# Performance work log

Measured on AMD Instinct MI355X. Metric: run time of the kernel, lower is better.

## Reference

```python
import jax, jax.numpy as jnp
import numpy as np

NEMB = 128
N_NODES = 8192
N_EDGES = 16384
N_STEMS = 4096
N_GRAPHS = 256
N_BLOCKS = 105       # BlockDictionary.n_unique_blocks
N_STEMTYPES = 32     # BlockDictionary.n_stem_types
OUT_PER_STEM = 105
OUT_PER_STOP = 1
NUM_CONV_STEPS = 12
SLOPE = 0.01         # nn.LeakyReLU default negative slope


def _act(v):
    return jax.nn.leaky_relu(v, SLOPE)


def setup_inputs() -> dict:
    key = jax.random.key(0)
    ks = jax.random.split(key, 32)
    def p(i, shape, fan_in):
        return jax.random.normal(ks[i], shape, jnp.float32) / np.sqrt(fan_in).astype(np.float32)
    D = NEMB
    inp = {
        "x": jax.random.randint(ks[0], (N_NODES,), 0, N_BLOCKS + 1),
        "stemtypes": jax.random.randint(ks[1], (N_STEMS,), 0, N_STEMTYPES + 1),
        "edge_attr": jax.random.randint(ks[2], (N_EDGES, 2), 0, N_STEMTYPES),
        "edge_index": jax.random.randint(ks[3], (2, N_EDGES), 0, N_NODES),
        "stem_node_idx": jax.random.randint(ks[4], (N_STEMS,), 0, N_NODES),
        "node_batch": jnp.sort(jax.random.randint(ks[5], (N_NODES,), 0, N_GRAPHS)),
        # embedding tables
        "emb_block": p(6, (N_BLOCKS + 1, D), D),
        "emb_stem": p(7, (N_STEMTYPES + 1, D), D),
        "emb_bond": p(8, (N_STEMTYPES, D), D),
        # block2emb MLP
        "b2e_w1": p(9, (D, D), D), "b2e_b1": p(10, (D,), D),
        "b2e_w2": p(11, (D, D), D), "b2e_b2": p(12, (D,), D),
        # NNConv root weight + bias (edge-nn is identity: nn.Sequential())
        "conv_root": p(13, (D, D), D), "conv_bias": p(14, (D,), D),
        # GRU (torch gate order r, z, n)
        "gru_w_ih": p(15, (3 * D, D), D), "gru_w_hh": p(16, (3 * D, D), D),
        "gru_b_ih": p(17, (3 * D,), D), "gru_b_hh": p(18, (3 * D,), D),
        # stem2pred MLP (in = 2*D)
        "s2p_w1": p(19, (D, 2 * D), 2 * D), "s2p_b1": p(20, (D,), 2 * D),
        "s2p_w2": p(21, (D, D), D), "s2p_b2": p(22, (D,), D),
        "s2p_w3": p(23, (OUT_PER_STEM, D), D), "s2p_b3": p(24, (OUT_PER_STEM,), D),
        # global2pred MLP
        "g2p_w1": p(25, (D, D), D), "g2p_b1": p(26, (D,), D),
        "g2p_w2": p(27, (OUT_PER_STOP, D), D), "g2p_b2": p(28, (OUT_PER_STOP,), D),
    }
    return inp


def reference(x, stemtypes, edge_attr, edge_index, stem_node_idx, node_batch,
              emb_block, emb_stem, emb_bond,
              b2e_w1, b2e_b1, b2e_w2, b2e_b2,
              conv_root, conv_bias,
              gru_w_ih, gru_w_hh, gru_b_ih, gru_b_hh,
              s2p_w1, s2p_b1, s2p_w2, s2p_b2, s2p_w3, s2p_b3,
              g2p_w1, g2p_b1, g2p_w2, g2p_b2):
    block_emb = emb_block[x]                          # [N, D]
    stem_emb = emb_stem[stemtypes]                    # [S, D]
    be = emb_bond[edge_attr]                          # [E, 2, D]
    # outer product -> per-edge [D_in, D_out] weight (matches view(-1, in, out))
    W_e = be[:, 0, :, None] * be[:, 1, None, :]       # [E, D, D]

    out = _act(block_emb @ b2e_w1.T + b2e_b1) @ b2e_w2.T + b2e_b2  # [N, D]
    h = out                                           # GRU hidden state

    src, dst = edge_index[0], edge_index[1]
    ones_e = jnp.ones((N_EDGES,), out.dtype)
    deg = jax.ops.segment_sum(ones_e, dst, num_segments=N_NODES)
    inv_deg = jnp.where(deg > 0, 1.0 / jnp.maximum(deg, 1.0), 0.0)[:, None]

    for _ in range(NUM_CONV_STEPS):
        # NNConv: mean_j (x_j @ W_e) + x @ root + bias, then LeakyReLU
        msg = jnp.einsum('ei,eij->ej', out[src], W_e)                  # [E, D]
        agg = jax.ops.segment_sum(msg, dst, num_segments=N_NODES) * inv_deg
        m = _act(agg + out @ conv_root + conv_bias)
        # single-layer GRU, seq_len = 1
        gi = m @ gru_w_ih.T + gru_b_ih
        gh = h @ gru_w_hh.T + gru_b_hh
        ir, iz, inn = jnp.split(gi, 3, axis=-1)
        hr, hz, hn = jnp.split(gh, 3, axis=-1)
        r = jax.nn.sigmoid(ir + hr)
        z = jax.nn.sigmoid(iz + hz)
        n = jnp.tanh(inn + r * hn)
        h = (1.0 - z) * n + z * h
        out = h

    stem_cat = jnp.concatenate([out[stem_node_idx], stem_emb], axis=1)  # [S, 2D]
    s = _act(stem_cat @ s2p_w1.T + s2p_b1)
    s = _act(s @ s2p_w2.T + s2p_b2)
    stem_pred = s @ s2p_w3.T + s2p_b3                                   # [S, out_per_stem]

    # global_mean_pool
    gsum = jax.ops.segment_sum(out, node_batch, num_segments=N_GRAPHS)
    gcnt = jax.ops.segment_sum(jnp.ones((N_NODES,), out.dtype), node_batch, num_segments=N_GRAPHS)
    gmean = gsum / jnp.maximum(gcnt, 1.0)[:, None]
    g = _act(gmean @ g2p_w1.T + g2p_b1)
    stop_pred = g @ g2p_w2.T + g2p_b2                                   # [G, out_per_stop]
    return stem_pred, stop_pred
```

## Files before the change

kernel.cpp:

```cpp
#include <hip/hip_runtime.h>
#include <math.h>

#define D 128
#define NNODES 8192
#define NEDGES 16384
#define NSTEMS 4096
#define NGRAPHS 256
#define NSTEPS 12
#define OPS 105
#define SLOPE 0.01f
#define MT 32
#define NB (NNODES / MT)
#define ECAP 512
#define LDA 136
#define LDA2 264
#define LDQ2 34
#define LDH 132

typedef _Float16 half_t;
typedef __attribute__((ext_vector_type(8))) _Float16 f16x8;
typedef __attribute__((ext_vector_type(4))) float f32x4;

__device__ __forceinline__ float leaky(float x) { return x > 0.f ? x : SLOPE * x; }
__device__ __forceinline__ float fast_sigmoid(float x) {
    return __builtin_amdgcn_rcpf(1.f + __expf(-x));
}
__device__ __forceinline__ float fast_tanh(float x) {
    float e = __expf(2.f * x);
    return 1.f - 2.f * __builtin_amdgcn_rcpf(e + 1.f);
}

__device__ __forceinline__ void gbar_arrive(int* bar, int sync_no) {
    __syncthreads();
    if (threadIdx.x == 0) {
        int grp = blockIdx.x >> 4;
        int old = __hip_atomic_fetch_add(&bar[grp * 32], 1,
                                         __ATOMIC_RELEASE, __HIP_MEMORY_SCOPE_AGENT);
        if (old == sync_no * 16 - 1) {
            int r = __hip_atomic_fetch_add(&bar[512], 1,
                                           __ATOMIC_RELEASE, __HIP_MEMORY_SCOPE_AGENT);
            if (r == sync_no * 16 - 1)
                __hip_atomic_store(&bar[544], sync_no,
                                   __ATOMIC_RELEASE, __HIP_MEMORY_SCOPE_AGENT);
        }
    }
}
__device__ __forceinline__ void gbar_wait(int* bar, int sync_no) {
    if (threadIdx.x == 0) {
        while (__hip_atomic_load(&bar[544], __ATOMIC_RELAXED,
                                 __HIP_MEMORY_SCOPE_AGENT) < sync_no)
            __builtin_amdgcn_s_sleep(1);
    }
    __syncthreads();
}

__global__ void k_setup(
    const float* __restrict__ root, const float* __restrict__ wih,
    const float* __restrict__ whh, const float* __restrict__ bond,
    const float* __restrict__ sw1, const float* __restrict__ sw2,
    const float* __restrict__ sw3, const float* __restrict__ bw1,
    const float* __restrict__ bw2, const float* __restrict__ gw1,
    half_t* __restrict__ rootP, half_t* __restrict__ WihP,
    half_t* __restrict__ WhhP, half_t* __restrict__ bondTP,
    half_t* __restrict__ s1P, half_t* __restrict__ s2P, half_t* __restrict__ s3P,
    half_t* __restrict__ w1P, half_t* __restrict__ w2P, half_t* __restrict__ bondQP,
    float* __restrict__ g1T, int* __restrict__ zeroi) {
    int idx = blockIdx.x * 256 + threadIdx.x;
    int which = blockIdx.y;
    if (which == 10) {
        if (idx < 128 * 128) {
            int r = idx >> 7, c = idx & 127;
            g1T[c * 128 + r] = gw1[idx];
        }
        return;
    }
    if (which == 11) {
        if (idx < 1024) zeroi[idx] = 0;
        return;
    }
    int KT = (which == 4) ? 8 : (which == 9) ? 1 : 4;
    int NT = (which == 1 || which == 2) ? 24 : (which == 3) ? 2 : (which == 6) ? 7 : 8;
    if (idx >= NT * KT * 512) return;
    int j = idx & 7;
    int L = (idx >> 3) & 63;
    int t = idx >> 9;
    int kt = t % KT, nt = t / KT;
    int k = kt * 32 + (L >> 4) * 8 + j;
    int n = nt * 16 + (L & 15);
    switch (which) {
        case 0: rootP[idx] = (half_t)root[k * D + n]; break;
        case 1: WihP[idx] = (half_t)wih[n * D + k]; break;
        case 2: WhhP[idx] = (half_t)whh[n * D + k]; break;
        case 3: bondTP[idx] = (half_t)bond[n * D + k]; break;
        case 4: s1P[idx] = (half_t)sw1[n * 256 + k]; break;
        case 5: s2P[idx] = (half_t)sw2[n * 128 + k]; break;
        case 6: s3P[idx] = (n < OPS) ? (half_t)sw3[n * 128 + k] : (half_t)0.f; break;
        case 7: w1P[idx] = (half_t)bw1[n * D + k]; break;
        case 8: w2P[idx] = (half_t)bw2[n * D + k]; break;
        case 9: bondQP[idx] = (half_t)bond[k * D + n]; break;
    }
}

__device__ __forceinline__ int lower_bound_dev(const int* a, int n, int v) {
    int lo = 0, hi = n;
    while (lo < hi) {
        int m = (lo + hi) >> 1;
        if (a[m] < v) lo = m + 1;
        else hi = m;
    }
    return lo;
}

__global__ __launch_bounds__(512, 2) void k_fused(
    const int* __restrict__ x, const float* __restrict__ embBlock,
    const half_t* __restrict__ w1P, const float* __restrict__ b1i,
    const half_t* __restrict__ w2P, const float* __restrict__ b2i,
    const half_t* __restrict__ rootP, const half_t* __restrict__ WihP,
    const half_t* __restrict__ WhhP, const half_t* __restrict__ bondTP,
    const half_t* __restrict__ bondQP,
    const float* __restrict__ cbias, const float* __restrict__ bih,
    const float* __restrict__ bhh,
    const int* __restrict__ eidx, const int* __restrict__ eattr,
    float* __restrict__ Pbuf0, float* __restrict__ Pbuf1,
    float* __restrict__ hF,
    const int* __restrict__ sni, const int* __restrict__ stypes,
    const float* __restrict__ embStem,
    const half_t* __restrict__ s1P, const float* __restrict__ sb1,
    const half_t* __restrict__ s2P, const float* __restrict__ sb2,
    const half_t* __restrict__ s3P, const float* __restrict__ sb3,
    const int* __restrict__ batch, const float* __restrict__ g1T,
    const float* __restrict__ gb1, const float* __restrict__ gw2,
    const float* __restrict__ gb2, float* __restrict__ dout,
    int* __restrict__ bar) {
    __shared__ __align__(16) half_t As[MT * LDA];
    __shared__ __align__(16) half_t Am[MT * LDA];
    __shared__ __align__(16) float Hs[MT * LDH];
    __shared__ __align__(16) float Q[MT * LDQ2];
    __shared__ __align__(16) int4 elist[ECAP];
    __shared__ int degs_s[MT];
    __shared__ int ecnt;

    const int tid = threadIdx.x;
    const int w = tid >> 6;
    const int lane = tid & 63;
    const int quad = lane >> 4;
    const int l16 = lane & 15;
    const int n0 = blockIdx.x * MT;
    const int c = w * 16 + l16;

    if (tid < MT) degs_s[tid] = 0;
    if (tid == 0) ecnt = 0;
    for (int i = tid; i < MT * LDQ2; i += 512) Q[i] = 0.f;
    __syncthreads();

    {
        int row = tid >> 4;
        int col = (tid & 15) * 8;
        const float* src = embBlock + (size_t)x[n0 + row] * D + col;
        float4 v0 = ((const float4*)src)[0];
        float4 v1 = ((const float4*)src)[1];
        f16x8 hv;
        hv[0] = (half_t)v0.x; hv[1] = (half_t)v0.y; hv[2] = (half_t)v0.z; hv[3] = (half_t)v0.w;
        hv[4] = (half_t)v1.x; hv[5] = (half_t)v1.y; hv[6] = (half_t)v1.z; hv[7] = (half_t)v1.w;
        *(f16x8*)&As[row * LDA + col] = hv;
    }
    {
        const int4* dst4 = (const int4*)(eidx + NEDGES);
        for (int e4 = tid; e4 < NEDGES / 4; e4 += 512) {
            int4 dd = dst4[e4];
            int eb = e4 * 4;
            int dv[4] = {dd.x, dd.y, dd.z, dd.w};
#pragma unroll
            for (int q2 = 0; q2 < 4; ++q2) {
                unsigned r = (unsigned)(dv[q2] - n0);
                if (r < MT) {
                    int slot = atomicAdd(&ecnt, 1);
                    atomicAdd(&degs_s[r], 1);
                    if (slot < ECAP) {
                        int e = eb + q2;
                        int2 aa = *(const int2*)(eattr + 2 * e);
                        elist[slot] = make_int4(eidx[e], aa.x, aa.y, (int)r);
                    }
                }
            }
        }
    }
    f16x8 rootB[4], ghB[12], giB[12], aggB, bondTB[4];
#pragma unroll
    for (int kt = 0; kt < 4; ++kt)
        rootB[kt] = *(const f16x8*)(rootP + (size_t)((w * 4 + kt) * 64 + lane) * 8);
#pragma unroll
    for (int kt = 0; kt < 4; ++kt)
#pragma unroll
        for (int g = 0; g < 3; ++g)
            ghB[g * 4 + kt] = *(const f16x8*)(WhhP + (size_t)(((g * 8 + w) * 4 + kt) * 64 + lane) * 8);
#pragma unroll
    for (int kt = 0; kt < 4; ++kt)
#pragma unroll
        for (int g = 0; g < 3; ++g)
            giB[g * 4 + kt] = *(const f16x8*)(WihP + (size_t)(((g * 8 + w) * 4 + kt) * 64 + lane) * 8);
    aggB = *(const f16x8*)(bondQP + (size_t)(w * 64 + lane) * 8);
    {
        const int ntb = w & 1;
#pragma unroll
        for (int kt = 0; kt < 4; ++kt)
            bondTB[kt] = *(const f16x8*)(bondTP + (size_t)((ntb * 4 + kt) * 64 + lane) * 8);
    }
    const float cb = cbias[c];
    const float bi0 = bih[c], bi1 = bih[D + c], bi2 = bih[2 * D + c];
    const float bh0 = bhh[c], bh1 = bhh[D + c], bh2 = bhh[2 * D + c];
    __syncthreads();

    int4 ep = make_int4(0, 0, 0, 0);
    float idg = 0.f;
    const int m = min(ecnt, ECAP);
    const bool have = (tid < m);
    if (have) {
        ep = elist[tid];
        idg = 1.0f / (float)degs_s[ep.w];
    }

    {
        f32x4 acc[2] = {{0.f, 0.f, 0.f, 0.f}, {0.f, 0.f, 0.f, 0.f}};
#pragma unroll
        for (int kt = 0; kt < 4; ++kt) {
            f16x8 b = *(const f16x8*)(w1P + (size_t)((w * 4 + kt) * 64 + lane) * 8);
            f16x8 a0 = *(const f16x8*)&As[(0 + l16) * LDA + kt * 32 + quad * 8];
            f16x8 a1 = *(const f16x8*)&As[(16 + l16) * LDA + kt * 32 + quad * 8];
            acc[0] = __builtin_amdgcn_mfma_f32_16x16x32_f16(a0, b, acc[0], 0, 0, 0);
            acc[1] = __builtin_amdgcn_mfma_f32_16x16x32_f16(a1, b, acc[1], 0, 0, 0);
        }
        float bb = b1i[c];
#pragma unroll
        for (int mt = 0; mt < 2; ++mt)
#pragma unroll
            for (int r = 0; r < 4; ++r)
                Am[(mt * 16 + quad * 4 + r) * LDA + c] = (half_t)leaky(acc[mt][r] + bb);
    }
    __syncthreads();
    {
        f32x4 acc[2] = {{0.f, 0.f, 0.f, 0.f}, {0.f, 0.f, 0.f, 0.f}};
#pragma unroll
        for (int kt = 0; kt < 4; ++kt) {
            f16x8 b = *(const f16x8*)(w2P + (size_t)((w * 4 + kt) * 64 + lane) * 8);
            f16x8 a0 = *(const f16x8*)&Am[(0 + l16) * LDA + kt * 32 + quad * 8];
            f16x8 a1 = *(const f16x8*)&Am[(16 + l16) * LDA + kt * 32 + quad * 8];
            acc[0] = __builtin_amdgcn_mfma_f32_16x16x32_f16(a0, b, acc[0], 0, 0, 0);
            acc[1] = __builtin_amdgcn_mfma_f32_16x16x32_f16(a1, b, acc[1], 0, 0, 0);
        }
        float bb = b2i[c];
#pragma unroll
        for (int mt = 0; mt < 2; ++mt)
#pragma unroll
            for (int r = 0; r < 4; ++r) {
                int row = mt * 16 + quad * 4 + r;
                float h = acc[mt][r] + bb;
                Hs[row * LDH + c] = h;
                As[row * LDA + c] = (half_t)h;
            }
    }
    __syncthreads();
    if (w < 4) {
        int mt = w >> 1;
        f32x4 acc = {0.f, 0.f, 0.f, 0.f};
#pragma unroll
        for (int kt = 0; kt < 4; ++kt) {
            f16x8 a = *(const f16x8*)&As[(mt * 16 + l16) * LDA + kt * 32 + quad * 8];
            acc = __builtin_amdgcn_mfma_f32_16x16x32_f16(a, bondTB[kt], acc, 0, 0, 0);
        }
#pragma unroll
        for (int r = 0; r < 4; ++r)
            __hip_atomic_store(
                &Pbuf0[(size_t)(n0 + mt * 16 + quad * 4 + r) * 32 + (w & 1) * 16 + l16],
                acc[r], __ATOMIC_RELAXED, __HIP_MEMORY_SCOPE_AGENT);
    }
    gbar_arrive(bar, 1);

    float* Pp = Pbuf0;
    float* Pn = Pbuf1;
    for (int step = 0; step < NSTEPS; ++step) {
        f32x4 ghA[2][3];
#pragma unroll
        for (int mt = 0; mt < 2; ++mt)
#pragma unroll
            for (int g = 0; g < 3; ++g) ghA[mt][g] = f32x4{0.f, 0.f, 0.f, 0.f};
#pragma unroll
        for (int kt = 0; kt < 4; ++kt) {
            f16x8 a0 = *(const f16x8*)&As[(0 + l16) * LDA + kt * 32 + quad * 8];
            f16x8 a1 = *(const f16x8*)&As[(16 + l16) * LDA + kt * 32 + quad * 8];
#pragma unroll
            for (int g = 0; g < 3; ++g) {
                ghA[0][g] = __builtin_amdgcn_mfma_f32_16x16x32_f16(a0, ghB[g * 4 + kt], ghA[0][g], 0, 0, 0);
                ghA[1][g] = __builtin_amdgcn_mfma_f32_16x16x32_f16(a1, ghB[g * 4 + kt], ghA[1][g], 0, 0, 0);
            }
        }
        gbar_wait(bar, step + 1);
        float wv = 0.f;
        if (have)
            wv = __hip_atomic_load(&Pp[(size_t)ep.x * 32 + ep.y],
                                   __ATOMIC_RELAXED, __HIP_MEMORY_SCOPE_AGENT) * idg;
        f32x4 convAcc[2] = {{0.f, 0.f, 0.f, 0.f}, {0.f, 0.f, 0.f, 0.f}};
#pragma unroll
        for (int kt = 0; kt < 4; ++kt) {
            f16x8 a0 = *(const f16x8*)&As[(0 + l16) * LDA + kt * 32 + quad * 8];
            f16x8 a1 = *(const f16x8*)&As[(16 + l16) * LDA + kt * 32 + quad * 8];
            convAcc[0] = __builtin_amdgcn_mfma_f32_16x16x32_f16(a0, rootB[kt], convAcc[0], 0, 0, 0);
            convAcc[1] = __builtin_amdgcn_mfma_f32_16x16x32_f16(a1, rootB[kt], convAcc[1], 0, 0, 0);
        }
        if (have) atomicAdd(&Q[ep.w * LDQ2 + ep.z], wv);
        __syncthreads();

#pragma unroll
        for (int mt = 0; mt < 2; ++mt) {
            const float* qrow = &Q[(mt * 16 + l16) * LDQ2 + quad * 8];
            f16x8 a;
#pragma unroll
            for (int jj = 0; jj < 8; ++jj) a[jj] = (half_t)qrow[jj];
            f32x4 acc = {0.f, 0.f, 0.f, 0.f};
            acc = __builtin_amdgcn_mfma_f32_16x16x32_f16(a, aggB, acc, 0, 0, 0);
#pragma unroll
            for (int r = 0; r < 4; ++r) {
                float mm = convAcc[mt][r] + cb + acc[r];
                Am[(mt * 16 + quad * 4 + r) * LDA + c] = (half_t)leaky(mm);
            }
        }
        __syncthreads();

        if (step < NSTEPS - 1)
            for (int i = tid; i < MT * LDQ2; i += 512) Q[i] = 0.f;
        f32x4 giA[2][3];
#pragma unroll
        for (int mt = 0; mt < 2; ++mt)
#pragma unroll
            for (int g = 0; g < 3; ++g) giA[mt][g] = f32x4{0.f, 0.f, 0.f, 0.f};
#pragma unroll
        for (int kt = 0; kt < 4; ++kt) {
            f16x8 a0 = *(const f16x8*)&Am[(0 + l16) * LDA + kt * 32 + quad * 8];
            f16x8 a1 = *(const f16x8*)&Am[(16 + l16) * LDA + kt * 32 + quad * 8];
#pragma unroll
            for (int g = 0; g < 3; ++g) {
                giA[0][g] = __builtin_amdgcn_mfma_f32_16x16x32_f16(a0, giB[g * 4 + kt], giA[0][g], 0, 0, 0);
                giA[1][g] = __builtin_amdgcn_mfma_f32_16x16x32_f16(a1, giB[g * 4 + kt], giA[1][g], 0, 0, 0);
            }
        }
#pragma unroll
        for (int mt = 0; mt < 2; ++mt) {
#pragma unroll
            for (int r = 0; r < 4; ++r) {
                int row = mt * 16 + quad * 4 + r;
                float rg = fast_sigmoid(giA[mt][0][r] + bi0 + ghA[mt][0][r] + bh0);
                float z = fast_sigmoid(giA[mt][1][r] + bi1 + ghA[mt][1][r] + bh1);
                float nn = fast_tanh(giA[mt][2][r] + bi2 + rg * (ghA[mt][2][r] + bh2));
                float hnew = (1.f - z) * nn + z * Hs[row * LDH + c];
                Hs[row * LDH + c] = hnew;
                As[row * LDA + c] = (half_t)hnew;
            }
        }
        __syncthreads();

        if (step < NSTEPS - 1) {
            if (w < 4) {
                int mt = w >> 1;
                f32x4 acc = {0.f, 0.f, 0.f, 0.f};
#pragma unroll
                for (int kt = 0; kt < 4; ++kt) {
                    f16x8 a = *(const f16x8*)&As[(mt * 16 + l16) * LDA + kt * 32 + quad * 8];
                    acc = __builtin_amdgcn_mfma_f32_16x16x32_f16(a, bondTB[kt], acc, 0, 0, 0);
                }
#pragma unroll
                for (int r = 0; r < 4; ++r)
                    __hip_atomic_store(
                        &Pn[(size_t)(n0 + mt * 16 + quad * 4 + r) * 32 + (w & 1) * 16 + l16],
                        acc[r], __ATOMIC_RELAXED, __HIP_MEMORY_SCOPE_AGENT);
            }
            gbar_arrive(bar, step + 2);
            float* tsw = Pp; Pp = Pn; Pn = tsw;
        }
    }

    half_t* cat = As;
    half_t* t1 = Am;
    half_t* t2 = Am + 16 * LDA;
    const int s0 = blockIdx.x * 16;
    {
        int row = tid >> 4;
        int col = (tid & 15) * 8;
        const unsigned long long* s8 = (const unsigned long long*)&Hs[row * LDH + col];
        unsigned long long* d8 = (unsigned long long*)(hF + (size_t)(n0 + row) * D + col);
#pragma unroll
        for (int q2 = 0; q2 < 4; ++q2)
            __hip_atomic_store(d8 + q2, s8[q2], __ATOMIC_RELAXED, __HIP_MEMORY_SCOPE_AGENT);
    }
    if (tid < 256) {
        int row = tid >> 4;
        int col = (tid & 15) * 8;
        const float* src = embStem + (size_t)stypes[s0 + row] * D + col;
        float4 v0 = ((const float4*)src)[0];
        float4 v1 = ((const float4*)src)[1];
        f16x8 hv;
        hv[0] = (half_t)v0.x; hv[1] = (half_t)v0.y; hv[2] = (half_t)v0.z; hv[3] = (half_t)v0.w;
        hv[4] = (half_t)v1.x; hv[5] = (half_t)v1.y; hv[6] = (half_t)v1.z; hv[7] = (half_t)v1.w;
        *(f16x8*)&cat[row * LDA2 + 128 + col] = hv;
    }
    gbar_arrive(bar, NSTEPS + 1);

    f32x4 accS = {0.f, 0.f, 0.f, 0.f};
#pragma unroll
    for (int kt = 4; kt < 8; ++kt) {
        f16x8 b = *(const f16x8*)(s1P + (size_t)((w * 8 + kt) * 64 + lane) * 8);
        f16x8 a = *(const f16x8*)&cat[l16 * LDA2 + kt * 32 + quad * 8];
        accS = __builtin_amdgcn_mfma_f32_16x16x32_f16(a, b, accS, 0, 0, 0);
    }
    gbar_wait(bar, NSTEPS + 1);

    if (tid < 256) {
        int row = tid >> 4;
        int col = (tid & 15) * 8;
        const float* src = hF + (size_t)sni[s0 + row] * D + col;
        float4 v0 = ((const float4*)src)[0];
        float4 v1 = ((const float4*)src)[1];
        f16x8 hv;
        hv[0] = (half_t)v0.x; hv[1] = (half_t)v0.y; hv[2] = (half_t)v0.z; hv[3] = (half_t)v0.w;
        hv[4] = (half_t)v1.x; hv[5] = (half_t)v1.y; hv[6] = (half_t)v1.z; hv[7] = (half_t)v1.w;
        *(f16x8*)&cat[row * LDA2 + col] = hv;
    }
    __syncthreads();
    {
#pragma unroll
        for (int kt = 0; kt < 4; ++kt) {
            f16x8 b = *(const f16x8*)(s1P + (size_t)((w * 8 + kt) * 64 + lane) * 8);
            f16x8 a = *(const f16x8*)&cat[l16 * LDA2 + kt * 32 + quad * 8];
            accS = __builtin_amdgcn_mfma_f32_16x16x32_f16(a, b, accS, 0, 0, 0);
        }
        float bb = sb1[c];
#pragma unroll
        for (int r = 0; r < 4; ++r)
            t1[(quad * 4 + r) * LDA + c] = (half_t)leaky(accS[r] + bb);
    }
    __syncthreads();
    {
        f32x4 acc = {0.f, 0.f, 0.f, 0.f};
#pragma unroll
        for (int kt = 0; kt < 4; ++kt) {
            f16x8 b = *(const f16x8*)(s2P + (size_t)((w * 4 + kt) * 64 + lane) * 8);
            f16x8 a = *(const f16x8*)&t1[l16 * LDA + kt * 32 + quad * 8];
            acc = __builtin_amdgcn_mfma_f32_16x16x32_f16(a, b, acc, 0, 0, 0);
        }
        float bb = sb2[c];
#pragma unroll
        for (int r = 0; r < 4; ++r)
            t2[(quad * 4 + r) * LDA + c] = (half_t)leaky(acc[r] + bb);
    }
    __syncthreads();
    if (w < 7) {
        f32x4 acc = {0.f, 0.f, 0.f, 0.f};
#pragma unroll
        for (int kt = 0; kt < 4; ++kt) {
            f16x8 b = *(const f16x8*)(s3P + (size_t)((w * 4 + kt) * 64 + lane) * 8);
            f16x8 a = *(const f16x8*)&t2[l16 * LDA + kt * 32 + quad * 8];
            acc = __builtin_amdgcn_mfma_f32_16x16x32_f16(a, b, acc, 0, 0, 0);
        }
        int j = w * 16 + l16;
        if (j < OPS) {
            float bb = sb3[j];
#pragma unroll
            for (int r = 0; r < 4; ++r)
                dout[(size_t)(s0 + quad * 4 + r) * OPS + j] = acc[r] + bb;
        }
    }

    {
        const int g = blockIdx.x;
        const int j = tid & 127;
        const int grp = tid >> 7;
        float* part = Q;
        float* mean_s = Q + 512;
        float* red = Q + 640;
        int lo = lower_bound_dev(batch, NNODES, g);
        int hi = lower_bound_dev(batch, NNODES, g + 1);
        float sum = 0.f;
        for (int n = lo + grp; n < hi; n += 4) sum += hF[(size_t)n * D + j];
        part[grp * 128 + j] = sum;
        __syncthreads();
        if (grp == 0) {
            float denom = (hi > lo) ? (float)(hi - lo) : 1.0f;
            mean_s[j] = (part[j] + part[128 + j] + part[256 + j] + part[384 + j]) / denom;
        }
        __syncthreads();
        float a = 0.f;
        for (int i = grp * 32; i < grp * 32 + 32; ++i) a += mean_s[i] * g1T[i * D + j];
        part[grp * 128 + j] = a;
        __syncthreads();
        if (grp == 0) {
            float aa = part[j] + part[128 + j] + part[256 + j] + part[384 + j] + gb1[j];
            red[j] = leaky(aa) * gw2[j];
        }
        __syncthreads();
        for (int off = 64; off > 0; off >>= 1) {
            if (tid < off) red[tid] += red[tid + off];
            __syncthreads();
        }
        if (tid == 0) dout[NSTEMS * OPS + g] = red[0] + gb2[0];
    }
}

extern "C" void kernel_launch(void* const* d_in, const int* in_sizes, int n_in,
                              void* d_out, int out_size, void* d_ws, size_t ws_size,
                              hipStream_t stream) {
    const int* x = (const int*)d_in[0];
    const int* stypes = (const int*)d_in[1];
    const int* eattr = (const int*)d_in[2];
    const int* eidx = (const int*)d_in[3];
    const int* sni = (const int*)d_in[4];
    const int* batch = (const int*)d_in[5];
    const float* embBlock = (const float*)d_in[6];
    const float* embStem = (const float*)d_in[7];
    const float* embBond = (const float*)d_in[8];
    const float* b2e_w1 = (const float*)d_in[9];
    const float* b2e_b1 = (const float*)d_in[10];
    const float* b2e_w2 = (const float*)d_in[11];
    const float* b2e_b2 = (const float*)d_in[12];
    const float* conv_root = (const float*)d_in[13];
    const float* conv_bias = (const float*)d_in[14];
    const float* gru_w_ih = (const float*)d_in[15];
    const float* gru_w_hh = (const float*)d_in[16];
    const float* gru_b_ih = (const float*)d_in[17];
    const float* gru_b_hh = (const float*)d_in[18];
    const float* s2p_w1 = (const float*)d_in[19];
    const float* s2p_b1 = (const float*)d_in[20];
    const float* s2p_w2 = (const float*)d_in[21];
    const float* s2p_b2 = (const float*)d_in[22];
    const float* s2p_w3 = (const float*)d_in[23];
    const float* s2p_b3 = (const float*)d_in[24];
    const float* g2p_w1 = (const float*)d_in[25];
    const float* g2p_b1 = (const float*)d_in[26];
    const float* g2p_w2 = (const float*)d_in[27];
    const float* g2p_b2 = (const float*)d_in[28];
    float* out_f = (float*)d_out;

    float* W = (float*)d_ws;
    size_t off = 0;
    auto alloc = [&](size_t words) {
        size_t o = off;
        off += (words + 3) & ~(size_t)3;
        return o;
    };
    float* hF = W + alloc(NNODES * D);
    float* P0 = W + alloc(NNODES * 32);
    float* P1 = W + alloc(NNODES * 32);
    half_t* rootP = (half_t*)(W + alloc(16384 / 2));
    half_t* WihP = (half_t*)(W + alloc(49152 / 2));
    half_t* WhhP = (half_t*)(W + alloc(49152 / 2));
    half_t* bondTP = (half_t*)(W + alloc(4096 / 2));
    half_t* s1P = (half_t*)(W + alloc(32768 / 2));
    half_t* s2P = (half_t*)(W + alloc(16384 / 2));
    half_t* s3P = (half_t*)(W + alloc(14336 / 2));
    half_t* w1P = (half_t*)(W + alloc(16384 / 2));
    half_t* w2P = (half_t*)(W + alloc(16384 / 2));
    half_t* bondQP = (half_t*)(W + alloc(4096 / 2));
    float* g1T = W + alloc(128 * 128);
    int* bar = (int*)(W + alloc(1024));

    k_setup<<<dim3(192, 12), 256, 0, stream>>>(
        conv_root, gru_w_ih, gru_w_hh, embBond, s2p_w1, s2p_w2, s2p_w3,
        b2e_w1, b2e_w2, g2p_w1,
        rootP, WihP, WhhP, bondTP, s1P, s2P, s3P, w1P, w2P, bondQP,
        g1T, bar);

    k_fused<<<NB, 512, 0, stream>>>(
        x, embBlock,
        w1P, b2e_b1, w2P, b2e_b2,
        rootP, WihP, WhhP, bondTP, bondQP,
        conv_bias, gru_b_ih, gru_b_hh,
        eidx, eattr,
        P0, P1, hF,
        sni, stypes, embStem,
        s1P, s2p_b1, s2P, s2p_b2, s3P, s2p_b3,
        batch, g1T, g2p_b1, g2p_w2, g2p_b2,
        out_f, bar);
}
```

Measured before the change: 219.8 us.

## Switch message passing from pull-gather to push-scatter with global atomics

Edges are now grouped by source node. Each block computes its nodes' projected messages in shared memory and atomically adds them, already scaled by inverse degree, into a double-buffered global aggregation array owned by the destination node. Each block then reads its own 32x32 aggregate slice contiguously and zeroes it for reuse. This replaces scattered per-edge remote loads after the barrier with atomics issued before the barrier, so the post-barrier critical path becomes one coalesced load. In exchange it adds an extra grid barrier to publish inverse degrees, more global atomic traffic, and a zeroing pass in setup.

```diff
diff --git a/kernel.cpp b/kernel.cpp
--- a/kernel.cpp
+++ b/kernel.cpp
@@ -64,7 +64,7 @@
     half_t* __restrict__ WhhP, half_t* __restrict__ bondTP,
     half_t* __restrict__ s1P, half_t* __restrict__ s2P, half_t* __restrict__ s3P,
     half_t* __restrict__ w1P, half_t* __restrict__ w2P, half_t* __restrict__ bondQP,
-    float* __restrict__ g1T, int* __restrict__ zeroi) {
+    float* __restrict__ g1T, int* __restrict__ zeroi, float* __restrict__ Qg) {
     int idx = blockIdx.x * 256 + threadIdx.x;
     int which = blockIdx.y;
     if (which == 10) {
@@ -76,6 +76,10 @@
     }
     if (which == 11) {
         if (idx < 1024) zeroi[idx] = 0;
+        return;
+    }
+    if (which == 12) {
+        for (int i = idx; i < 2 * NNODES * 32; i += 192 * 256) Qg[i] = 0.f;
         return;
     }
     int KT = (which == 4) ? 8 : (which == 9) ? 1 : 4;
@@ -121,7 +125,7 @@
     const float* __restrict__ cbias, const float* __restrict__ bih,
     const float* __restrict__ bhh,
     const int* __restrict__ eidx, const int* __restrict__ eattr,
-    float* __restrict__ Pbuf0, float* __restrict__ Pbuf1,
+    float* __restrict__ Qg, float* __restrict__ invDegG,
     float* __restrict__ hF,
     const int* __restrict__ sni, const int* __restrict__ stypes,
     const float* __restrict__ embStem,
@@ -135,7 +139,7 @@
     __shared__ __align__(16) half_t As[MT * LDA];
     __shared__ __align__(16) half_t Am[MT * LDA];
     __shared__ __align__(16) float Hs[MT * LDH];
-    __shared__ __align__(16) float Q[MT * LDQ2];
+    __shared__ __align__(16) float QPs[MT * LDQ2];
     __shared__ __align__(16) int4 elist[ECAP];
     __shared__ int degs_s[MT];
     __shared__ int ecnt;
@@ -150,7 +154,6 @@
 
     if (tid < MT) degs_s[tid] = 0;
     if (tid == 0) ecnt = 0;
-    for (int i = tid; i < MT * LDQ2; i += 512) Q[i] = 0.f;
     __syncthreads();
 
     {
@@ -165,21 +168,25 @@
         *(f16x8*)&As[row * LDA + col] = hv;
     }
     {
-        const int4* dst4 = (const int4*)(eidx + NEDGES);
+        const int4* src4p = (const int4*)eidx;
+        const int4* dst4p = (const int4*)(eidx + NEDGES);
         for (int e4 = tid; e4 < NEDGES / 4; e4 += 512) {
-            int4 dd = dst4[e4];
+            int4 ss = src4p[e4];
+            int4 dd = dst4p[e4];
             int eb = e4 * 4;
+            int sv[4] = {ss.x, ss.y, ss.z, ss.w};
             int dv[4] = {dd.x, dd.y, dd.z, dd.w};
 #pragma unroll
             for (int q2 = 0; q2 < 4; ++q2) {
-                unsigned r = (unsigned)(dv[q2] - n0);
-                if (r < MT) {
+                unsigned rd = (unsigned)(dv[q2] - n0);
+                if (rd < MT) atomicAdd(&degs_s[rd], 1);
+                unsigned rs = (unsigned)(sv[q2] - n0);
+                if (rs < MT) {
                     int slot = atomicAdd(&ecnt, 1);
-                    atomicAdd(&degs_s[r], 1);
                     if (slot < ECAP) {
                         int e = eb + q2;
                         int2 aa = *(const int2*)(eattr + 2 * e);
-                        elist[slot] = make_int4(eidx[e], aa.x, aa.y, (int)r);
+                        elist[slot] = make_int4((int)rs, aa.x, aa.y, dv[q2]);
                     }
                 }
             }
@@ -211,14 +218,16 @@
     const float bh0 = bhh[c], bh1 = bhh[D + c], bh2 = bhh[2 * D + c];
     __syncthreads();
 
+    if (tid < MT) {
+        int dg = degs_s[tid];
+        __hip_atomic_store(&invDegG[n0 + tid], dg > 0 ? 1.0f / (float)dg : 0.0f,
+                           __ATOMIC_RELAXED, __HIP_MEMORY_SCOPE_AGENT);
+    }
     int4 ep = make_int4(0, 0, 0, 0);
-    float idg = 0.f;
     const int m = min(ecnt, ECAP);
     const bool have = (tid < m);
-    if (have) {
-        ep = elist[tid];
-        idg = 1.0f / (float)degs_s[ep.w];
-    }
+    if (have) ep = elist[tid];
+    gbar_arrive(bar, 1);
 
     {
         f32x4 acc[2] = {{0.f, 0.f, 0.f, 0.f}, {0.f, 0.f, 0.f, 0.f}};
@@ -260,6 +269,10 @@
             }
     }
     __syncthreads();
+    gbar_wait(bar, 1);
+    float idg = 0.f;
+    if (have)
+        idg = __hip_atomic_load(&invDegG[ep.w], __ATOMIC_RELAXED, __HIP_MEMORY_SCOPE_AGENT);
     if (w < 4) {
         int mt = w >> 1;
         f32x4 acc = {0.f, 0.f, 0.f, 0.f};
@@ -270,14 +283,13 @@
         }
 #pragma unroll
         for (int r = 0; r < 4; ++r)
-            __hip_atomic_store(
-                &Pbuf0[(size_t)(n0 + mt * 16 + quad * 4 + r) * 32 + (w & 1) * 16 + l16],
-                acc[r], __ATOMIC_RELAXED, __HIP_MEMORY_SCOPE_AGENT);
-    }
-    gbar_arrive(bar, 1);
-
-    float* Pp = Pbuf0;
-    float* Pn = Pbuf1;
+            QPs[(mt * 16 + quad * 4 + r) * LDQ2 + (w & 1) * 16 + l16] = acc[r];
+    }
+    __syncthreads();
+    if (have)
+        atomicAdd(&Qg[(size_t)ep.w * 32 + ep.z], QPs[ep.x * LDQ2 + ep.y] * idg);
+    gbar_arrive(bar, 2);
+
     for (int step = 0; step < NSTEPS; ++step) {
         f32x4 ghA[2][3];
 #pragma unroll
@@ -294,11 +306,11 @@
                 ghA[1][g] = __builtin_amdgcn_mfma_f32_16x16x32_f16(a1, ghB[g * 4 + kt], ghA[1][g], 0, 0, 0);
             }
         }
-        gbar_wait(bar, step + 1);
-        float wv = 0.f;
-        if (have)
-            wv = __hip_atomic_load(&Pp[(size_t)ep.x * 32 + ep.y],
-                                   __ATOMIC_RELAXED, __HIP_MEMORY_SCOPE_AGENT) * idg;
+        gbar_wait(bar, step + 2);
+        float* Qc = Qg + (size_t)(step & 1) * (NNODES * 32) + (size_t)n0 * 32;
+        unsigned long long qv =
+            __hip_atomic_load((unsigned long long*)(Qc + tid * 2),
+                              __ATOMIC_RELAXED, __HIP_MEMORY_SCOPE_AGENT);
         f32x4 convAcc[2] = {{0.f, 0.f, 0.f, 0.f}, {0.f, 0.f, 0.f, 0.f}};
 #pragma unroll
         for (int kt = 0; kt < 4; ++kt) {
@@ -307,12 +319,20 @@
             convAcc[0] = __builtin_amdgcn_mfma_f32_16x16x32_f16(a0, rootB[kt], convAcc[0], 0, 0, 0);
             convAcc[1] = __builtin_amdgcn_mfma_f32_16x16x32_f16(a1, rootB[kt], convAcc[1], 0, 0, 0);
         }
-        if (have) atomicAdd(&Q[ep.w * LDQ2 + ep.z], wv);
+        {
+            union { unsigned long long u; float f[2]; } qu;
+            qu.u = qv;
+            int row = tid >> 4, col = (tid & 15) * 2;
+            QPs[row * LDQ2 + col] = qu.f[0];
+            QPs[row * LDQ2 + col + 1] = qu.f[1];
+            __hip_atomic_store((unsigned long long*)(Qc + tid * 2), 0ULL,
+                               __ATOMIC_RELAXED, __HIP_MEMORY_SCOPE_AGENT);
+        }
         __syncthreads();
 
 #pragma unroll
         for (int mt = 0; mt < 2; ++mt) {
-            const float* qrow = &Q[(mt * 16 + l16) * LDQ2 + quad * 8];
+            const float* qrow = &QPs[(mt * 16 + l16) * LDQ2 + quad * 8];
             f16x8 a;
 #pragma unroll
             for (int jj = 0; jj < 8; ++jj) a[jj] = (half_t)qrow[jj];
@@ -326,8 +346,6 @@
         }
         __syncthreads();
 
-        if (step < NSTEPS - 1)
-            for (int i = tid; i < MT * LDQ2; i += 512) Q[i] = 0.f;
         f32x4 giA[2][3];
 #pragma unroll
         for (int mt = 0; mt < 2; ++mt)
@@ -369,12 +387,14 @@
                 }
 #pragma unroll
                 for (int r = 0; r < 4; ++r)
-                    __hip_atomic_store(
-                        &Pn[(size_t)(n0 + mt * 16 + quad * 4 + r) * 32 + (w & 1) * 16 + l16],
-                        acc[r], __ATOMIC_RELAXED, __HIP_MEMORY_SCOPE_AGENT);
+                    QPs[(mt * 16 + quad * 4 + r) * LDQ2 + (w & 1) * 16 + l16] = acc[r];
             }
-            gbar_arrive(bar, step + 2);
-            float* tsw = Pp; Pp = Pn; Pn = tsw;
+            __syncthreads();
+            if (have)
+                atomicAdd(&Qg[(size_t)((step + 1) & 1) * (NNODES * 32) +
+                              (size_t)ep.w * 32 + ep.z],
+                          QPs[ep.x * LDQ2 + ep.y] * idg);
+            gbar_arrive(bar, step + 3);
         }
     }
 
@@ -402,7 +422,7 @@
         hv[4] = (half_t)v1.x; hv[5] = (half_t)v1.y; hv[6] = (half_t)v1.z; hv[7] = (half_t)v1.w;
         *(f16x8*)&cat[row * LDA2 + 128 + col] = hv;
     }
-    gbar_arrive(bar, NSTEPS + 1);
+    gbar_arrive(bar, NSTEPS + 2);
 
     f32x4 accS = {0.f, 0.f, 0.f, 0.f};
 #pragma unroll
@@ -411,7 +431,7 @@
         f16x8 a = *(const f16x8*)&cat[l16 * LDA2 + kt * 32 + quad * 8];
         accS = __builtin_amdgcn_mfma_f32_16x16x32_f16(a, b, accS, 0, 0, 0);
     }
-    gbar_wait(bar, NSTEPS + 1);
+    gbar_wait(bar, NSTEPS + 2);
 
     if (tid < 256) {
         int row = tid >> 4;
@@ -473,9 +493,9 @@
         const int g = blockIdx.x;
         const int j = tid & 127;
         const int grp = tid >> 7;
-        float* part = Q;
-        float* mean_s = Q + 512;
-        float* red = Q + 640;
+        float* part = QPs;
+        float* mean_s = QPs + 512;
+        float* red = QPs + 640;
         int lo = lower_bound_dev(batch, NNODES, g);
         int hi = lower_bound_dev(batch, NNODES, g + 1);
         float sum = 0.f;
@@ -546,8 +566,8 @@
         return o;
     };
     float* hF = W + alloc(NNODES * D);
-    float* P0 = W + alloc(NNODES * 32);
-    float* P1 = W + alloc(NNODES * 32);
+    float* Qg = W + alloc(2 * NNODES * 32);
+    float* invDegG = W + alloc(NNODES);
     half_t* rootP = (half_t*)(W + alloc(16384 / 2));
     half_t* WihP = (half_t*)(W + alloc(49152 / 2));
     half_t* WhhP = (half_t*)(W + alloc(49152 / 2));
@@ -561,11 +581,11 @@
     float* g1T = W + alloc(128 * 128);
     int* bar = (int*)(W + alloc(1024));
 
-    k_setup<<<dim3(192, 12), 256, 0, stream>>>(
+    k_setup<<<dim3(192, 13), 256, 0, stream>>>(
         conv_root, gru_w_ih, gru_w_hh, embBond, s2p_w1, s2p_w2, s2p_w3,
         b2e_w1, b2e_w2, g2p_w1,
         rootP, WihP, WhhP, bondTP, s1P, s2P, s3P, w1P, w2P, bondQP,
-        g1T, bar);
+        g1T, bar, Qg);
 
     k_fused<<<NB, 512, 0, stream>>>(
         x, embBlock,
@@ -573,7 +593,7 @@
         rootP, WihP, WhhP, bondTP, bondQP,
         conv_bias, gru_b_ih, gru_b_hh,
         eidx, eattr,
-        P0, P1, hF,
+        Qg, invDegG, hF,
         sni, stypes, embStem,
         s1P, s2p_b1, s2P, s2p_b2, s3P, s2p_b3,
         batch, g1T, g2p_b1, g2p_w2, g2p_b2,
```

After: 226.8 us. +3.2%, slower.
